# Performance work log

Measured on AMD Instinct MI355X. Metric: run time of the kernel, lower is better.

## Reference

```python
import jax, jax.numpy as jnp
import numpy as np

B, N, F_IN, F_OUT = 8, 2048, 256, 256
NEG_SLOPE = 0.2
EPS = 1e-7


def setup_inputs() -> dict:
    key = jax.random.key(0)
    k1, k2, k3, k4, k5 = jax.random.split(key, 5)
    x = jax.random.normal(k1, (B, N, F_IN), dtype=jnp.float32)
    # A is a 0/1 adjacency mask used as float in the module
    A = jax.random.bernoulli(k2, 0.5, (B, N, N)).astype(jnp.float32)
    # W: xavier_normal_ init, shape [in_features, out_features]
    W = jax.random.normal(k3, (F_IN, F_OUT), dtype=jnp.float32) * np.sqrt(2.0 / (F_IN + F_OUT))
    # attention_mechanism: Linear(2*F_OUT, 1) -> weight vector [2*F_OUT], scalar bias
    bound = 1.0 / np.sqrt(2 * F_OUT)
    a_w = jax.random.uniform(k4, (2 * F_OUT,), dtype=jnp.float32, minval=-bound, maxval=bound)
    a_b = jax.random.uniform(k5, (), dtype=jnp.float32, minval=-bound, maxval=bound)
    return {"A": A, "x": x, "W": W, "a_w": a_w, "a_b": a_b}


def reference(A, x, W, a_w, a_b):
    # Wh = x @ W : [B, N, F_OUT]
    Wh = jnp.einsum('bnf,fo->bno', x, W)
    # Linear([Wh_i ; Wh_j]) == Wh_i @ a_w[:F] + Wh_j @ a_w[F:] + b  (no O(N^2 F) concat)
    s_src = Wh @ a_w[:F_OUT]   # [B, N] contribution of row index i
    s_dst = Wh @ a_w[F_OUT:]   # [B, N] contribution of col index j
    e = s_src[:, :, None] + s_dst[:, None, :] + a_b  # [B, N, N]
    e = jnp.where(e > 0, e, NEG_SLOPE * e)           # leaky_relu(0.2)
    # masked softmax over dim=1 (as in the original module)
    exps = jnp.exp(e) * A
    sums = jnp.sum(exps, axis=1, keepdims=True) + EPS
    attn = exps / sums                                # [B, N, N]
    return jnp.einsum('bij,bjo->bio', attn, Wh)       # [B, N, F_OUT]
```

## Files before the change

### kernel.cpp

```cpp
#include <hip/hip_runtime.h>
#include <hip/hip_bf16.h>

#define NN 2048
#define BB 8
#define FD 256
#define NEG_SLOPE 0.2f
#define EPSV 1e-7f
#define PSTR 36

typedef __bf16 bf16x8 __attribute__((ext_vector_type(8)));
typedef __bf16 bf16x4 __attribute__((ext_vector_type(4)));
typedef float f32x4 __attribute__((ext_vector_type(4)));

__device__ __forceinline__ void gload16(const __bf16* g, __bf16* l) {
    __builtin_amdgcn_global_load_lds((const __attribute__((address_space(1))) unsigned int*)g,
                                     (__attribute__((address_space(3))) unsigned int*)l,
                                     16, 0, 0);
}

__global__ __launch_bounds__(256) void k1_prep(const float* __restrict__ W,
                                               __bf16* __restrict__ WT) {
    int idx = blockIdx.x * 256 + threadIdx.x;
    int o = idx >> 8, f = idx & 255;
    WT[idx] = (__bf16)W[f * FD + o];
}

__global__ __launch_bounds__(256) void k2_whgemm(const float* __restrict__ x,
                                                 const __bf16* __restrict__ WT,
                                                 float* __restrict__ Wh) {
    const int wave = threadIdx.x >> 6;
    const int lane = threadIdx.x & 63;
    const int row0 = blockIdx.x * 32 + (wave >> 1) * 16;
    const int ohalf = (wave & 1) * 128;
    const int m = lane & 15;
    const int quad = lane >> 4;
    const int row = row0 + m;
    const float* xrow = x + (size_t)row * FD + quad * 8;

    f32x4 acc[8];
#pragma unroll
    for (int n = 0; n < 8; ++n) acc[n] = (f32x4){0.f, 0.f, 0.f, 0.f};

    for (int k0 = 0; k0 < FD; k0 += 32) {
        float4 xa = *(const float4*)(xrow + k0);
        float4 xb = *(const float4*)(xrow + k0 + 4);
        bf16x8 af;
        af[0] = (__bf16)xa.x; af[1] = (__bf16)xa.y; af[2] = (__bf16)xa.z; af[3] = (__bf16)xa.w;
        af[4] = (__bf16)xb.x; af[5] = (__bf16)xb.y; af[6] = (__bf16)xb.z; af[7] = (__bf16)xb.w;
#pragma unroll
        for (int n = 0; n < 8; ++n) {
            int o = ohalf + n * 16 + m;
            bf16x8 bf = *(const bf16x8*)(WT + o * FD + k0 + quad * 8);
            acc[n] = __builtin_amdgcn_mfma_f32_16x16x32_bf16(af, bf, acc[n], 0, 0, 0);
        }
    }
#pragma unroll
    for (int n = 0; n < 8; ++n) {
        int o = ohalf + n * 16 + m;
#pragma unroll
        for (int r = 0; r < 4; ++r) {
            Wh[(size_t)(row0 + quad * 4 + r) * FD + o] = acc[n][r];
        }
    }
}

__global__ __launch_bounds__(256) void k3_scores(const float* __restrict__ Wh,
                                                 const float* __restrict__ a_w,
                                                 float* __restrict__ s_src,
                                                 float* __restrict__ s_dst) {
    int wave = threadIdx.x >> 6, lane = threadIdx.x & 63;
    int row = blockIdx.x * 4 + wave;
    float4 wv = *(const float4*)(Wh + (size_t)row * FD + lane * 4);
    float4 a0 = *(const float4*)(a_w + lane * 4);
    float4 a1 = *(const float4*)(a_w + FD + lane * 4);
    float d0 = wv.x * a0.x + wv.y * a0.y + wv.z * a0.z + wv.w * a0.w;
    float d1 = wv.x * a1.x + wv.y * a1.y + wv.z * a1.z + wv.w * a1.w;
#pragma unroll
    for (int off = 32; off; off >>= 1) {
        d0 += __shfl_down(d0, off, 64);
        d1 += __shfl_down(d1, off, 64);
    }
    if (lane == 0) { s_src[row] = d0; s_dst[row] = d1; }
}

__global__ __launch_bounds__(256) void k4_den(const float* __restrict__ A,
                                              const float* __restrict__ s_src,
                                              const float* __restrict__ s_dst,
                                              const float* __restrict__ a_bp,
                                              float* __restrict__ den_part) {
    const int blk = blockIdx.x;
    const int b = blk & 7;
    const int jhalf = (blk >> 3) & 1;
    const int isp = blk >> 4;
    const int i0 = isp * 32;
    const int j = jhalf * 1024 + threadIdx.x * 4;
    __shared__ float ss[32];
    if (threadIdx.x < 32) ss[threadIdx.x] = s_src[b * NN + i0 + threadIdx.x] + a_bp[0];
    __syncthreads();
    float4 sd = *(const float4*)(s_dst + b * NN + j);
    float ax = 0.f, ay = 0.f, az = 0.f, aw = 0.f;
    const float* Ap = A + ((size_t)b * NN + i0) * NN + j;
#pragma unroll 8
    for (int i = 0; i < 32; ++i) {
        float4 a = *(const float4*)(Ap + (size_t)i * NN);
        float si = ss[i];
        float e0 = si + sd.x; e0 = e0 > 0.f ? e0 : NEG_SLOPE * e0;
        float e1 = si + sd.y; e1 = e1 > 0.f ? e1 : NEG_SLOPE * e1;
        float e2 = si + sd.z; e2 = e2 > 0.f ? e2 : NEG_SLOPE * e2;
        float e3 = si + sd.w; e3 = e3 > 0.f ? e3 : NEG_SLOPE * e3;
        ax += a.x * __expf(e0);
        ay += a.y * __expf(e1);
        az += a.z * __expf(e2);
        aw += a.w * __expf(e3);
    }
    float4 r = (float4){ax, ay, az, aw};
    *(float4*)(den_part + (size_t)isp * (BB * NN) + b * NN + j) = r;
}

__global__ __launch_bounds__(256) void k5_wht(const float* __restrict__ Wh,
                                              const float* __restrict__ den_part,
                                              __bf16* __restrict__ WhT) {
    const int b = blockIdx.z;
    const int j0 = blockIdx.x * 64;
    const int o0 = blockIdx.y * 64;
    __shared__ float tile[64][65];
    __shared__ float invd[64];
    if (threadIdx.x < 64) {
        float s = 0.f;
        const float* dp = den_part + b * NN + j0 + threadIdx.x;
#pragma unroll 8
        for (int sI = 0; sI < 64; ++sI) s += dp[(size_t)sI * (BB * NN)];
        invd[threadIdx.x] = 1.f / (s + EPSV);
    }
    __syncthreads();
    int jr = threadIdx.x >> 4, oc = (threadIdx.x & 15) * 4;
#pragma unroll
    for (int p = 0; p < 4; ++p) {
        int jj = jr + p * 16;
        float4 v = *(const float4*)(Wh + (size_t)(b * NN + j0 + jj) * FD + o0 + oc);
        float s = invd[jj];
        tile[jj][oc + 0] = v.x * s;
        tile[jj][oc + 1] = v.y * s;
        tile[jj][oc + 2] = v.z * s;
        tile[jj][oc + 3] = v.w * s;
    }
    __syncthreads();
    int ow = threadIdx.x >> 4, jc = (threadIdx.x & 15) * 4;
#pragma unroll
    for (int p = 0; p < 4; ++p) {
        int o = ow + p * 16;
        bf16x4 wv;
        wv[0] = (__bf16)tile[jc + 0][o];
        wv[1] = (__bf16)tile[jc + 1][o];
        wv[2] = (__bf16)tile[jc + 2][o];
        wv[3] = (__bf16)tile[jc + 3][o];
        *(bf16x4*)(WhT + (size_t)(b * FD + o0 + o) * NN + j0 + jc) = wv;
    }
}

__global__ __launch_bounds__(256) void k6_out(const float* __restrict__ A,
                                              const __bf16* __restrict__ WhT,
                                              const float* __restrict__ s_src,
                                              const float* __restrict__ s_dst,
                                              const float* __restrict__ a_bp,
                                              float* __restrict__ out) {
    __shared__ __bf16 Pt[2][32 * PSTR];
    __shared__ __bf16 Bt[2][256 * 32];
    const int blk = blockIdx.x;
    const int b = blk & 7;
    const int itile = blk >> 3;
    const int i0 = itile * 32;
    const int t = threadIdx.x;
    const int w = t >> 6, lane = t & 63;
    const int m = lane & 15, quad = lane >> 4;

    const int prow = t >> 3, pj = (t & 7) * 4;
    const float ssr = s_src[b * NN + i0 + prow] + a_bp[0];
    const float* Abase = A + ((size_t)(b * NN + i0 + prow)) * NN + pj;
    const float* sdbase = s_dst + b * NN + pj;
    __bf16* Pw = &Pt[0][0] + prow * PSTR + pj;
    const int pstep = 32 * PSTR;

    const int srow = t >> 2, schunk = t & 3;
    const __bf16* gB = WhT + ((size_t)(b * FD + srow)) * NN + schunk * 8;
    __bf16* lB = &Bt[0][(w * 16) * 32];
    const int lstepB = 256 * 32;

    float4 a0 = *(const float4*)(Abase);
    float4 q0 = *(const float4*)(sdbase);
#pragma unroll
    for (int c = 0; c < 4; ++c) gload16(gB + (size_t)(c * 64) * NN, lB + c * 64 * 32);

#define BUILD_P(dstbuf)                                                          \
    {                                                                            \
        bf16x4 pv; float e;                                                      \
        e = ssr + q0.x; e = e > 0.f ? e : NEG_SLOPE * e; pv[0] = (__bf16)(a0.x * __expf(e)); \
        e = ssr + q0.y; e = e > 0.f ? e : NEG_SLOPE * e; pv[1] = (__bf16)(a0.y * __expf(e)); \
        e = ssr + q0.z; e = e > 0.f ? e : NEG_SLOPE * e; pv[2] = (__bf16)(a0.z * __expf(e)); \
        e = ssr + q0.w; e = e > 0.f ? e : NEG_SLOPE * e; pv[3] = (__bf16)(a0.w * __expf(e)); \
        *(bf16x4*)(Pw + (dstbuf) * pstep) = pv;                                  \
    }

    BUILD_P(0)

    f32x4 acc[2][4];
#pragma unroll
    for (int r = 0; r < 2; ++r)
#pragma unroll
        for (int n = 0; n < 4; ++n) acc[r][n] = (f32x4){0.f, 0.f, 0.f, 0.f};

    const __bf16* Pr = &Pt[0][m * PSTR + quad * 8];
    const __bf16* Br = &Bt[0][(w * 64 + m) * 32 + quad * 8];

    for (int kk = 0; kk < 64; ++kk) {
        __syncthreads();
        const int cur = kk & 1, nb = cur ^ 1;
        if (kk < 63) {
#pragma unroll
            for (int c = 0; c < 4; ++c)
                gload16(gB + (size_t)(c * 64) * NN + (kk + 1) * 32, lB + nb * lstepB + c * 64 * 32);
            a0 = *(const float4*)(Abase + (kk + 1) * 32);
            q0 = *(const float4*)(sdbase + (kk + 1) * 32);
        }
        const __bf16* Pk = Pr + cur * pstep;
        const __bf16* Bk = Br + cur * lstepB;
        bf16x8 af[2];
        af[0] = *(const bf16x8*)(Pk);
        af[1] = *(const bf16x8*)(Pk + 16 * PSTR);
#pragma unroll
        for (int n = 0; n < 4; ++n) {
            bf16x8 bfr = *(const bf16x8*)(Bk + n * 16 * 32);
#pragma unroll
            for (int r = 0; r < 2; ++r)
                acc[r][n] = __builtin_amdgcn_mfma_f32_16x16x32_bf16(af[r], bfr, acc[r][n], 0, 0, 0);
        }
        if (kk < 63) BUILD_P(nb)
    }

#pragma unroll
    for (int r = 0; r < 2; ++r) {
#pragma unroll
        for (int n = 0; n < 4; ++n) {
            int o = w * 64 + n * 16 + m;
#pragma unroll
            for (int rr = 0; rr < 4; ++rr) {
                int row = i0 + r * 16 + quad * 4 + rr;
                out[((size_t)b * NN + row) * FD + o] = acc[r][n][rr];
            }
        }
    }
#undef BUILD_P
}

extern "C" void kernel_launch(void* const* d_in, const int* in_sizes, int n_in,
                              void* d_out, int out_size, void* d_ws, size_t ws_size,
                              hipStream_t stream) {
    const float* A   = (const float*)d_in[0];
    const float* x   = (const float*)d_in[1];
    const float* W   = (const float*)d_in[2];
    const float* a_w = (const float*)d_in[3];
    const float* a_b = (const float*)d_in[4];
    float* out = (float*)d_out;

    char* ws = (char*)d_ws;
    __bf16* WT      = (__bf16*)ws;
    float*  Wh      = (float*)(ws + 131072);
    __bf16* WhT     = (__bf16*)(ws + 16908288);
    float*  s_src   = (float*)(ws + 25296896);
    float*  s_dst   = (float*)(ws + 25362432);
    float*  den_part= (float*)(ws + 25427968);

    k1_prep<<<256, 256, 0, stream>>>(W, WT);
    k2_whgemm<<<512, 256, 0, stream>>>(x, WT, Wh);
    k3_scores<<<4096, 256, 0, stream>>>(Wh, a_w, s_src, s_dst);
    k4_den<<<1024, 256, 0, stream>>>(A, s_src, s_dst, a_b, den_part);
    k5_wht<<<dim3(32, 4, 8), 256, 0, stream>>>(Wh, den_part, WhT);
    k6_out<<<512, 256, 0, stream>>>(A, WhT, s_src, s_dst, a_b, out);
}
```

Baseline: 306.4 us.

## Retile attention-output GEMM into LDS-free 64x64 tiles with direct global fragment loads

The output kernel changes from 32-row by 256-column tiles staged through double-buffered LDS to 64-row by 64-column tiles. Each wave now loads its adjacency and score values straight into registers and builds its own bf16 P fragment. It also loads the WhT B fragments directly from global memory, which removes the LDS traffic and block barriers and doubles the block count. In exchange, each A row and its exponentials are read and recomputed four times, once per output-column tile. B fragment loads are also uncoalesced strided 16-byte reads.

New measurement: 426.1 us. +39.1%, slower.

```diff
diff --git a/kernel.cpp b/kernel.cpp
--- a/kernel.cpp
+++ b/kernel.cpp
@@ -6,17 +6,10 @@
 #define FD 256
 #define NEG_SLOPE 0.2f
 #define EPSV 1e-7f
-#define PSTR 36
 
 typedef __bf16 bf16x8 __attribute__((ext_vector_type(8)));
 typedef __bf16 bf16x4 __attribute__((ext_vector_type(4)));
 typedef float f32x4 __attribute__((ext_vector_type(4)));
-
-__device__ __forceinline__ void gload16(const __bf16* g, __bf16* l) {
-    __builtin_amdgcn_global_load_lds((const __attribute__((address_space(1))) unsigned int*)g,
-                                     (__attribute__((address_space(3))) unsigned int*)l,
-                                     16, 0, 0);
-}
 
 __global__ __launch_bounds__(256) void k1_prep(const float* __restrict__ W,
                                                __bf16* __restrict__ WT) {
@@ -164,92 +157,71 @@
                                               const float* __restrict__ s_dst,
                                               const float* __restrict__ a_bp,
                                               float* __restrict__ out) {
-    __shared__ __bf16 Pt[2][32 * PSTR];
-    __shared__ __bf16 Bt[2][256 * 32];
     const int blk = blockIdx.x;
     const int b = blk & 7;
-    const int itile = blk >> 3;
-    const int i0 = itile * 32;
+    const int r_ = blk >> 3;
+    const int rowtile = r_ & 31;
+    const int otile = r_ >> 5;
+    const int i0 = rowtile * 64;
+    const int o0 = otile * 64;
     const int t = threadIdx.x;
     const int w = t >> 6, lane = t & 63;
     const int m = lane & 15, quad = lane >> 4;
 
-    const int prow = t >> 3, pj = (t & 7) * 4;
-    const float ssr = s_src[b * NN + i0 + prow] + a_bp[0];
-    const float* Abase = A + ((size_t)(b * NN + i0 + prow)) * NN + pj;
-    const float* sdbase = s_dst + b * NN + pj;
-    __bf16* Pw = &Pt[0][0] + prow * PSTR + pj;
-    const int pstep = 32 * PSTR;
-
-    const int srow = t >> 2, schunk = t & 3;
-    const __bf16* gB = WhT + ((size_t)(b * FD + srow)) * NN + schunk * 8;
-    __bf16* lB = &Bt[0][(w * 16) * 32];
-    const int lstepB = 256 * 32;
-
-    float4 a0 = *(const float4*)(Abase);
-    float4 q0 = *(const float4*)(sdbase);
-#pragma unroll
-    for (int c = 0; c < 4; ++c) gload16(gB + (size_t)(c * 64) * NN, lB + c * 64 * 32);
-
-#define BUILD_P(dstbuf)                                                          \
-    {                                                                            \
-        bf16x4 pv; float e;                                                      \
-        e = ssr + q0.x; e = e > 0.f ? e : NEG_SLOPE * e; pv[0] = (__bf16)(a0.x * __expf(e)); \
-        e = ssr + q0.y; e = e > 0.f ? e : NEG_SLOPE * e; pv[1] = (__bf16)(a0.y * __expf(e)); \
-        e = ssr + q0.z; e = e > 0.f ? e : NEG_SLOPE * e; pv[2] = (__bf16)(a0.z * __expf(e)); \
-        e = ssr + q0.w; e = e > 0.f ? e : NEG_SLOPE * e; pv[3] = (__bf16)(a0.w * __expf(e)); \
-        *(bf16x4*)(Pw + (dstbuf) * pstep) = pv;                                  \
-    }
-
-    BUILD_P(0)
-
-    f32x4 acc[2][4];
-#pragma unroll
-    for (int r = 0; r < 2; ++r)
-#pragma unroll
-        for (int n = 0; n < 4; ++n) acc[r][n] = (f32x4){0.f, 0.f, 0.f, 0.f};
-
-    const __bf16* Pr = &Pt[0][m * PSTR + quad * 8];
-    const __bf16* Br = &Bt[0][(w * 64 + m) * 32 + quad * 8];
+    const int row = i0 + w * 16 + m;
+    const float ssr = s_src[b * NN + row] + a_bp[0];
+    const float* Arow = A + ((size_t)b * NN + row) * NN + quad * 8;
+    const float* sdp = s_dst + b * NN + quad * 8;
+    const __bf16* Bb = WhT + (size_t)(b * FD + o0 + m) * NN + quad * 8;
+
+    f32x4 acc[4];
+#pragma unroll
+    for (int n = 0; n < 4; ++n) acc[n] = (f32x4){0.f, 0.f, 0.f, 0.f};
+
+    float4 a0 = *(const float4*)(Arow);
+    float4 a1 = *(const float4*)(Arow + 4);
+    float4 s0 = *(const float4*)(sdp);
+    float4 s1 = *(const float4*)(sdp + 4);
 
     for (int kk = 0; kk < 64; ++kk) {
-        __syncthreads();
-        const int cur = kk & 1, nb = cur ^ 1;
+        bf16x8 bf0 = *(const bf16x8*)(Bb + (size_t)(0 * 16) * NN + kk * 32);
+        bf16x8 bf1 = *(const bf16x8*)(Bb + (size_t)(1 * 16) * NN + kk * 32);
+        bf16x8 bf2 = *(const bf16x8*)(Bb + (size_t)(2 * 16) * NN + kk * 32);
+        bf16x8 bf3 = *(const bf16x8*)(Bb + (size_t)(3 * 16) * NN + kk * 32);
+        float4 ca0 = a0, ca1 = a1, cs0 = s0, cs1 = s1;
         if (kk < 63) {
-#pragma unroll
-            for (int c = 0; c < 4; ++c)
-                gload16(gB + (size_t)(c * 64) * NN + (kk + 1) * 32, lB + nb * lstepB + c * 64 * 32);
-            a0 = *(const float4*)(Abase + (kk + 1) * 32);
-            q0 = *(const float4*)(sdbase + (kk + 1) * 32);
-        }
-        const __bf16* Pk = Pr + cur * pstep;
-        const __bf16* Bk = Br + cur * lstepB;
-        bf16x8 af[2];
-        af[0] = *(const bf16x8*)(Pk);
-        af[1] = *(const bf16x8*)(Pk + 16 * PSTR);
-#pragma unroll
-        for (int n = 0; n < 4; ++n) {
-            bf16x8 bfr = *(const bf16x8*)(Bk + n * 16 * 32);
-#pragma unroll
-            for (int r = 0; r < 2; ++r)
-                acc[r][n] = __builtin_amdgcn_mfma_f32_16x16x32_bf16(af[r], bfr, acc[r][n], 0, 0, 0);
-        }
-        if (kk < 63) BUILD_P(nb)
-    }
-
-#pragma unroll
-    for (int r = 0; r < 2; ++r) {
-#pragma unroll
-        for (int n = 0; n < 4; ++n) {
-            int o = w * 64 + n * 16 + m;
-#pragma unroll
-            for (int rr = 0; rr < 4; ++rr) {
-                int row = i0 + r * 16 + quad * 4 + rr;
-                out[((size_t)b * NN + row) * FD + o] = acc[r][n][rr];
-            }
-        }
-    }
-#undef BUILD_P
+            const float* An = Arow + (kk + 1) * 32;
+            const float* Sn = sdp + (kk + 1) * 32;
+            a0 = *(const float4*)(An);
+            a1 = *(const float4*)(An + 4);
+            s0 = *(const float4*)(Sn);
+            s1 = *(const float4*)(Sn + 4);
+        }
+        bf16x8 af;
+        float e;
+        e = ssr + cs0.x; e = e > 0.f ? e : NEG_SLOPE * e; af[0] = (__bf16)(ca0.x * __expf(e));
+        e = ssr + cs0.y; e = e > 0.f ? e : NEG_SLOPE * e; af[1] = (__bf16)(ca0.y * __expf(e));
+        e = ssr + cs0.z; e = e > 0.f ? e : NEG_SLOPE * e; af[2] = (__bf16)(ca0.z * __expf(e));
+        e = ssr + cs0.w; e = e > 0.f ? e : NEG_SLOPE * e; af[3] = (__bf16)(ca0.w * __expf(e));
+        e = ssr + cs1.x; e = e > 0.f ? e : NEG_SLOPE * e; af[4] = (__bf16)(ca1.x * __expf(e));
+        e = ssr + cs1.y; e = e > 0.f ? e : NEG_SLOPE * e; af[5] = (__bf16)(ca1.y * __expf(e));
+        e = ssr + cs1.z; e = e > 0.f ? e : NEG_SLOPE * e; af[6] = (__bf16)(ca1.z * __expf(e));
+        e = ssr + cs1.w; e = e > 0.f ? e : NEG_SLOPE * e; af[7] = (__bf16)(ca1.w * __expf(e));
+        acc[0] = __builtin_amdgcn_mfma_f32_16x16x32_bf16(af, bf0, acc[0], 0, 0, 0);
+        acc[1] = __builtin_amdgcn_mfma_f32_16x16x32_bf16(af, bf1, acc[1], 0, 0, 0);
+        acc[2] = __builtin_amdgcn_mfma_f32_16x16x32_bf16(af, bf2, acc[2], 0, 0, 0);
+        acc[3] = __builtin_amdgcn_mfma_f32_16x16x32_bf16(af, bf3, acc[3], 0, 0, 0);
+    }
+
+#pragma unroll
+    for (int n = 0; n < 4; ++n) {
+        int o = o0 + n * 16 + m;
+#pragma unroll
+        for (int rr = 0; rr < 4; ++rr) {
+            int orow = i0 + w * 16 + quad * 4 + rr;
+            out[((size_t)b * NN + orow) * FD + o] = acc[n][rr];
+        }
+    }
 }
 
 extern "C" void kernel_launch(void* const* d_in, const int* in_sizes, int n_in,
@@ -275,5 +247,5 @@
     k3_scores<<<4096, 256, 0, stream>>>(Wh, a_w, s_src, s_dst);
     k4_den<<<1024, 256, 0, stream>>>(A, s_src, s_dst, a_b, den_part);
     k5_wht<<<dim3(32, 4, 8), 256, 0, stream>>>(Wh, den_part, WhT);
-    k6_out<<<512, 256, 0, stream>>>(A, WhT, s_src, s_dst, a_b, out);
-}
+    k6_out<<<1024, 256, 0, stream>>>(A, WhT, s_src, s_dst, a_b, out);
+}
```

## Fuse score dot-products into Wh GEMM and widen output kernel to 512 threads

Applied to the files above, without the earlier changes.

Computes s_src and s_dst inside the Wh GEMM epilogue from the MFMA accumulators, using shuffle and LDS reductions, so the separate scores kernel and its re-read of Wh go away. The output kernel moves to 512 threads with 8 waves in a 2x4 grid, each wave owning a 16x64 tile. Each thread now builds half as many P entries and issues half as many async loads per step. This adds latency hiding through more waves per block, at the cost of fewer MFMAs per wave and more block-wide synchronisation per k-step.

After: 303.6 us. About the same (-0.9%).

```diff
diff --git a/kernel.cpp b/kernel.cpp
--- a/kernel.cpp
+++ b/kernel.cpp
@@ -10,6 +10,7 @@
 
 typedef __bf16 bf16x8 __attribute__((ext_vector_type(8)));
 typedef __bf16 bf16x4 __attribute__((ext_vector_type(4)));
+typedef __bf16 bf16x2 __attribute__((ext_vector_type(2)));
 typedef float f32x4 __attribute__((ext_vector_type(4)));
 
 __device__ __forceinline__ void gload16(const __bf16* g, __bf16* l) {
@@ -27,7 +28,10 @@
 
 __global__ __launch_bounds__(256) void k2_whgemm(const float* __restrict__ x,
                                                  const __bf16* __restrict__ WT,
-                                                 float* __restrict__ Wh) {
+                                                 const float* __restrict__ a_w,
+                                                 float* __restrict__ Wh,
+                                                 float* __restrict__ s_src,
+                                                 float* __restrict__ s_dst) {
     const int wave = threadIdx.x >> 6;
     const int lane = threadIdx.x & 63;
     const int row0 = blockIdx.x * 32 + (wave >> 1) * 16;
@@ -62,25 +66,43 @@
             Wh[(size_t)(row0 + quad * 4 + r) * FD + o] = acc[n][r];
         }
     }
-}
-
-__global__ __launch_bounds__(256) void k3_scores(const float* __restrict__ Wh,
-                                                 const float* __restrict__ a_w,
-                                                 float* __restrict__ s_src,
-                                                 float* __restrict__ s_dst) {
-    int wave = threadIdx.x >> 6, lane = threadIdx.x & 63;
-    int row = blockIdx.x * 4 + wave;
-    float4 wv = *(const float4*)(Wh + (size_t)row * FD + lane * 4);
-    float4 a0 = *(const float4*)(a_w + lane * 4);
-    float4 a1 = *(const float4*)(a_w + FD + lane * 4);
-    float d0 = wv.x * a0.x + wv.y * a0.y + wv.z * a0.z + wv.w * a0.w;
-    float d1 = wv.x * a1.x + wv.y * a1.y + wv.z * a1.z + wv.w * a1.w;
-#pragma unroll
-    for (int off = 32; off; off >>= 1) {
-        d0 += __shfl_down(d0, off, 64);
-        d1 += __shfl_down(d1, off, 64);
-    }
-    if (lane == 0) { s_src[row] = d0; s_dst[row] = d1; }
+
+    float psrc[4] = {0.f, 0.f, 0.f, 0.f};
+    float pdst[4] = {0.f, 0.f, 0.f, 0.f};
+#pragma unroll
+    for (int n = 0; n < 8; ++n) {
+        int o = ohalf + n * 16 + m;
+        float awS = a_w[o], awD = a_w[FD + o];
+#pragma unroll
+        for (int r = 0; r < 4; ++r) {
+            psrc[r] += acc[n][r] * awS;
+            pdst[r] += acc[n][r] * awD;
+        }
+    }
+#pragma unroll
+    for (int off = 1; off <= 8; off <<= 1) {
+#pragma unroll
+        for (int r = 0; r < 4; ++r) {
+            psrc[r] += __shfl_xor(psrc[r], off, 64);
+            pdst[r] += __shfl_xor(pdst[r], off, 64);
+        }
+    }
+    __shared__ float sS[2][2][16], sD[2][2][16];
+    if (m == 0) {
+        int rp = wave >> 1, oh = wave & 1;
+#pragma unroll
+        for (int r = 0; r < 4; ++r) {
+            sS[rp][oh][quad * 4 + r] = psrc[r];
+            sD[rp][oh][quad * 4 + r] = pdst[r];
+        }
+    }
+    __syncthreads();
+    if (threadIdx.x < 32) {
+        int rp = threadIdx.x >> 4, idx = threadIdx.x & 15;
+        int orow = blockIdx.x * 32 + rp * 16 + idx;
+        s_src[orow] = sS[rp][0][idx] + sS[rp][1][idx];
+        s_dst[orow] = sD[rp][0][idx] + sD[rp][1][idx];
+    }
 }
 
 __global__ __launch_bounds__(256) void k4_den(const float* __restrict__ A,
@@ -158,7 +180,7 @@
     }
 }
 
-__global__ __launch_bounds__(256) void k6_out(const float* __restrict__ A,
+__global__ __launch_bounds__(512) void k6_out(const float* __restrict__ A,
                                               const __bf16* __restrict__ WhT,
                                               const float* __restrict__ s_src,
                                               const float* __restrict__ s_dst,
@@ -173,80 +195,69 @@
     const int t = threadIdx.x;
     const int w = t >> 6, lane = t & 63;
     const int m = lane & 15, quad = lane >> 4;
-
-    const int prow = t >> 3, pj = (t & 7) * 4;
+    const int wrow = w >> 2, wcol = w & 3;
+
+    const int prow = t >> 4, pjc = (t & 15) * 2;
     const float ssr = s_src[b * NN + i0 + prow] + a_bp[0];
-    const float* Abase = A + ((size_t)(b * NN + i0 + prow)) * NN + pj;
-    const float* sdbase = s_dst + b * NN + pj;
-    __bf16* Pw = &Pt[0][0] + prow * PSTR + pj;
+    const float* Abase = A + ((size_t)(b * NN + i0 + prow)) * NN + pjc;
+    const float* sdbase = s_dst + b * NN + pjc;
+    __bf16* Pw = &Pt[0][0] + prow * PSTR + pjc;
     const int pstep = 32 * PSTR;
 
     const int srow = t >> 2, schunk = t & 3;
     const __bf16* gB = WhT + ((size_t)(b * FD + srow)) * NN + schunk * 8;
-    __bf16* lB = &Bt[0][(w * 16) * 32];
+    __bf16* lB = &Bt[0][0] + (w * 16) * 32;
     const int lstepB = 256 * 32;
 
-    float4 a0 = *(const float4*)(Abase);
-    float4 q0 = *(const float4*)(sdbase);
-#pragma unroll
-    for (int c = 0; c < 4; ++c) gload16(gB + (size_t)(c * 64) * NN, lB + c * 64 * 32);
+    float2 a0 = *(const float2*)(Abase);
+    float2 q0 = *(const float2*)(sdbase);
+    gload16(gB, lB);
+    gload16(gB + (size_t)128 * NN, lB + 128 * 32);
 
 #define BUILD_P(dstbuf)                                                          \
     {                                                                            \
-        bf16x4 pv; float e;                                                      \
+        bf16x2 pv; float e;                                                      \
         e = ssr + q0.x; e = e > 0.f ? e : NEG_SLOPE * e; pv[0] = (__bf16)(a0.x * __expf(e)); \
         e = ssr + q0.y; e = e > 0.f ? e : NEG_SLOPE * e; pv[1] = (__bf16)(a0.y * __expf(e)); \
-        e = ssr + q0.z; e = e > 0.f ? e : NEG_SLOPE * e; pv[2] = (__bf16)(a0.z * __expf(e)); \
-        e = ssr + q0.w; e = e > 0.f ? e : NEG_SLOPE * e; pv[3] = (__bf16)(a0.w * __expf(e)); \
-        *(bf16x4*)(Pw + (dstbuf) * pstep) = pv;                                  \
+        *(bf16x2*)(Pw + (dstbuf) * pstep) = pv;                                  \
     }
 
     BUILD_P(0)
 
-    f32x4 acc[2][4];
-#pragma unroll
-    for (int r = 0; r < 2; ++r)
-#pragma unroll
-        for (int n = 0; n < 4; ++n) acc[r][n] = (f32x4){0.f, 0.f, 0.f, 0.f};
-
-    const __bf16* Pr = &Pt[0][m * PSTR + quad * 8];
-    const __bf16* Br = &Bt[0][(w * 64 + m) * 32 + quad * 8];
+    f32x4 acc[4];
+#pragma unroll
+    for (int n = 0; n < 4; ++n) acc[n] = (f32x4){0.f, 0.f, 0.f, 0.f};
+
+    const __bf16* Pr = &Pt[0][0] + (wrow * 16 + m) * PSTR + quad * 8;
+    const __bf16* Br = &Bt[0][0] + (wcol * 64 + m) * 32 + quad * 8;
 
     for (int kk = 0; kk < 64; ++kk) {
         __syncthreads();
         const int cur = kk & 1, nb = cur ^ 1;
         if (kk < 63) {
-#pragma unroll
-            for (int c = 0; c < 4; ++c)
-                gload16(gB + (size_t)(c * 64) * NN + (kk + 1) * 32, lB + nb * lstepB + c * 64 * 32);
-            a0 = *(const float4*)(Abase + (kk + 1) * 32);
-            q0 = *(const float4*)(sdbase + (kk + 1) * 32);
+            gload16(gB + (kk + 1) * 32, lB + nb * lstepB);
+            gload16(gB + (size_t)128 * NN + (kk + 1) * 32, lB + nb * lstepB + 128 * 32);
+            a0 = *(const float2*)(Abase + (kk + 1) * 32);
+            q0 = *(const float2*)(sdbase + (kk + 1) * 32);
         }
         const __bf16* Pk = Pr + cur * pstep;
         const __bf16* Bk = Br + cur * lstepB;
-        bf16x8 af[2];
-        af[0] = *(const bf16x8*)(Pk);
-        af[1] = *(const bf16x8*)(Pk + 16 * PSTR);
+        bf16x8 af = *(const bf16x8*)(Pk);
 #pragma unroll
         for (int n = 0; n < 4; ++n) {
             bf16x8 bfr = *(const bf16x8*)(Bk + n * 16 * 32);
-#pragma unroll
-            for (int r = 0; r < 2; ++r)
-                acc[r][n] = __builtin_amdgcn_mfma_f32_16x16x32_bf16(af[r], bfr, acc[r][n], 0, 0, 0);
+            acc[n] = __builtin_amdgcn_mfma_f32_16x16x32_bf16(af, bfr, acc[n], 0, 0, 0);
         }
         if (kk < 63) BUILD_P(nb)
     }
 
 #pragma unroll
-    for (int r = 0; r < 2; ++r) {
-#pragma unroll
-        for (int n = 0; n < 4; ++n) {
-            int o = w * 64 + n * 16 + m;
-#pragma unroll
-            for (int rr = 0; rr < 4; ++rr) {
-                int row = i0 + r * 16 + quad * 4 + rr;
-                out[((size_t)b * NN + row) * FD + o] = acc[r][n][rr];
-            }
+    for (int n = 0; n < 4; ++n) {
+        int o = wcol * 64 + n * 16 + m;
+#pragma unroll
+        for (int rr = 0; rr < 4; ++rr) {
+            int orow = i0 + wrow * 16 + quad * 4 + rr;
+            out[((size_t)b * NN + orow) * FD + o] = acc[n][rr];
         }
     }
 #undef BUILD_P
@@ -271,9 +282,8 @@
     float*  den_part= (float*)(ws + 25427968);
 
     k1_prep<<<256, 256, 0, stream>>>(W, WT);
-    k2_whgemm<<<512, 256, 0, stream>>>(x, WT, Wh);
-    k3_scores<<<4096, 256, 0, stream>>>(Wh, a_w, s_src, s_dst);
+    k2_whgemm<<<512, 256, 0, stream>>>(x, WT, a_w, Wh, s_src, s_dst);
     k4_den<<<1024, 256, 0, stream>>>(A, s_src, s_dst, a_b, den_part);
     k5_wht<<<dim3(32, 4, 8), 256, 0, stream>>>(Wh, den_part, WhT);
-    k6_out<<<512, 256, 0, stream>>>(A, WhT, s_src, s_dst, a_b, out);
-}
+    k6_out<<<512, 512, 0, stream>>>(A, WhT, s_src, s_dst, a_b, out);
+}
```
